# Kernel tuning notes

Hardware: AMD Instinct MI355X
Metric: run time of the kernel (lower is better)

The kernel has to match this reference:

```python
import jax, jax.numpy as jnp
import numpy as np

B, S, D = 2, 2048, 1024
H, HD = 16, 64  # num_attention_heads, attention_head_size


def setup_inputs() -> dict:
    key = jax.random.key(0)
    ks = jax.random.split(key, 8)
    std = 0.02
    return {
        "hidden_states": jax.random.normal(ks[0], (B, S, D), dtype=jnp.float32),
        "attention_mask": jnp.zeros((B, 1, 1, S), dtype=jnp.float32),
        "Wq": jax.random.normal(ks[1], (D, D), dtype=jnp.float32) * std,
        "bq": jnp.zeros((D,), dtype=jnp.float32),
        "Wk": jax.random.normal(ks[2], (D, D), dtype=jnp.float32) * std,
        "bk": jnp.zeros((D,), dtype=jnp.float32),
        "Wv": jax.random.normal(ks[3], (D, D), dtype=jnp.float32) * std,
        "bv": jnp.zeros((D,), dtype=jnp.float32),
    }


def reference(hidden_states, attention_mask, Wq, bq, Wk, bk, Wv, bv):
    b, s, d = hidden_states.shape

    def split_heads(x):  # [b,s,D] -> [b,H,s,HD]
        return x.reshape(b, s, H, HD).transpose(0, 2, 1, 3)

    q = split_heads(hidden_states @ Wq + bq)
    k = split_heads(hidden_states @ Wk + bk)
    v = split_heads(hidden_states @ Wv + bv)

    scores = jnp.einsum("bhqd,bhkd->bhqk", q, k) / jnp.sqrt(jnp.float32(HD))
    scores = scores + attention_mask  # additive mask, broadcast [b,1,1,s]
    probs = jax.nn.softmax(scores, axis=-1)  # dropout is identity at inference
    ctx = jnp.einsum("bhqk,bhkd->bhqd", probs, v)
    out = ctx.transpose(0, 2, 1, 3).reshape(b, s, d)
    return out
```

## Files before the change

### kernel.cpp

```cpp
#include <hip/hip_runtime.h>
#include <math.h>

#define CB 2
#define CS 2048
#define CD 1024
#define CH 16
#define CHD 64
#define CM (CB*CS)

#define QSCALE 0.18033688f
#define LOG2E  1.44269504f
#define BLOG   40.0f

typedef unsigned short u16;
using bf16x8 = __attribute__((ext_vector_type(8))) short;
using u16x8  = __attribute__((ext_vector_type(8))) unsigned short;
using f32x4  = __attribute__((ext_vector_type(4))) float;

__device__ __forceinline__ u16 f2bf(float f) {
    unsigned int u = __float_as_uint(f);
    u = (u + 0x7FFFu + ((u >> 16) & 1u)) >> 16;
    return (u16)u;
}

__device__ __forceinline__ unsigned cvt_pk_bf16(float lo, float hi) {
    unsigned r;
    asm("v_cvt_pk_bf16_f32 %0, %1, %2" : "=v"(r) : "v"(lo), "v"(hi));
    return r;
}

__device__ __forceinline__ void load_lds16(const u16* g, u16* l) {
    __builtin_amdgcn_global_load_lds(
        (const __attribute__((address_space(1))) unsigned int*)g,
        (__attribute__((address_space(3))) unsigned int*)l, 16, 0, 0);
}

__global__ __launch_bounds__(256)
void convert_x(const float* __restrict__ X, u16* __restrict__ Xb)
{
    size_t i = ((size_t)blockIdx.x * 256 + threadIdx.x) * 8;
    float4 v0 = *(const float4*)(X + i);
    float4 v1 = *(const float4*)(X + i + 4);
    u16x8 o;
    o[0] = f2bf(v0.x); o[1] = f2bf(v0.y); o[2] = f2bf(v0.z); o[3] = f2bf(v0.w);
    o[4] = f2bf(v1.x); o[5] = f2bf(v1.y); o[6] = f2bf(v1.z); o[7] = f2bf(v1.w);
    *(u16x8*)(Xb + i) = o;
}

__global__ __launch_bounds__(256)
void convert_wt(const float* __restrict__ Wq, const float* __restrict__ Wk,
                const float* __restrict__ Wv, u16* __restrict__ Wt)
{
    const int z = blockIdx.z;
    const float* W = (z == 0) ? Wq : (z == 1) ? Wk : Wv;
    const float sc = (z == 0) ? QSCALE : 1.0f;
    u16* Wo = Wt + (size_t)z * CD * CD;

    __shared__ u16 T[64][72];
    const int k0 = blockIdx.x << 6;
    const int n0 = blockIdx.y << 6;
    const int tid = threadIdx.x;

    #pragma unroll
    for (int it = 0; it < 4; ++it) {
        int r = (tid >> 4) + (it << 4);
        int c = (tid & 15) << 2;
        float4 v = *(const float4*)(W + (size_t)(k0 + r) * CD + n0 + c);
        T[c + 0][r] = f2bf(v.x * sc);
        T[c + 1][r] = f2bf(v.y * sc);
        T[c + 2][r] = f2bf(v.z * sc);
        T[c + 3][r] = f2bf(v.w * sc);
    }
    __syncthreads();
    #pragma unroll
    for (int it = 0; it < 2; ++it) {
        int cc = tid + (it << 8);
        int n  = cc >> 3;
        int ch = (cc & 7) << 3;
        *(uint4*)(Wo + (size_t)(n0 + n) * CD + k0 + ch) = *(const uint4*)&T[n][ch];
    }
}

__global__ __launch_bounds__(256, 3)
void qkv_gemm_mfma(const u16* __restrict__ Xb, const u16* __restrict__ Wt,
                   const float* __restrict__ bq, const float* __restrict__ bk,
                   const float* __restrict__ bv,
                   u16* __restrict__ Qb, u16* __restrict__ Kb,
                   u16* __restrict__ Vt)
{
    const int z = blockIdx.z;
    const u16* W = Wt + (size_t)z * CD * CD;
    const float* bias = (z == 0) ? bq : (z == 1) ? bk : bv;
    const float bscale = (z == 0) ? QSCALE : 1.0f;

    __shared__ u16 smem[16384];
    u16* As = smem;
    u16* Bs = smem + 8192;

    const int tid  = threadIdx.x;
    const int w    = tid >> 6;
    const int l    = tid & 63;
    const int l15  = l & 15;
    const int quad = l >> 4;
    const int wm   = w >> 1;
    const int wn   = w & 1;

    const int row0 = blockIdx.x << 7;
    const int n0   = blockIdx.y << 7;

    f32x4 acc[4][4];
    #pragma unroll
    for (int mi = 0; mi < 4; ++mi)
        #pragma unroll
        for (int nt = 0; nt < 4; ++nt)
            acc[mi][nt] = (f32x4){0.f, 0.f, 0.f, 0.f};

    const u16* Ag = Xb + (size_t)row0 * CD;
    const u16* Bg = W  + (size_t)n0   * CD;
    const int lr8 = l >> 3;
    const int ls  = l & 7;
    const int lg  = (ls ^ lr8) << 3;
    const int q7  = l15 & 7;

    for (int k0 = 0; k0 < CD; k0 += 64) {
        __syncthreads();
        #pragma unroll
        for (int i = 0; i < 4; ++i) {
            int r = w * 32 + 8 * i + lr8;
            load_lds16(Ag + (size_t)r * CD + k0 + lg, As + (size_t)(w * 32 + 8 * i) * 64);
            load_lds16(Bg + (size_t)r * CD + k0 + lg, Bs + (size_t)(w * 32 + 8 * i) * 64);
        }
        __syncthreads();

        #pragma unroll
        for (int kk = 0; kk < 2; ++kk) {
            bf16x8 af[4], bfr[4];
            #pragma unroll
            for (int mi = 0; mi < 4; ++mi)
                af[mi] = *(const bf16x8*)
                    &As[(wm * 64 + mi * 16 + l15) * 64 + (((kk * 4 + quad) ^ q7) << 3)];
            #pragma unroll
            for (int nt = 0; nt < 4; ++nt)
                bfr[nt] = *(const bf16x8*)
                    &Bs[(wn * 64 + nt * 16 + l15) * 64 + (((kk * 4 + quad) ^ q7) << 3)];
            #pragma unroll
            for (int mi = 0; mi < 4; ++mi)
                #pragma unroll
                for (int nt = 0; nt < 4; ++nt)
                    acc[mi][nt] = __builtin_amdgcn_mfma_f32_16x16x32_bf16(
                        af[mi], bfr[nt], acc[mi][nt], 0, 0, 0);
        }
    }

    __syncthreads();

    if (z < 2) {
        u16* Og = (z == 0) ? Qb : Kb;
        float bb[4];
        #pragma unroll
        for (int nt = 0; nt < 4; ++nt)
            bb[nt] = bias[n0 + wn * 64 + nt * 16 + l15] * bscale;

        u16 (*Ct)[136] = (u16(*)[136])smem;
        #pragma unroll
        for (int mh = 0; mh < 2; ++mh) {
            if (wm == mh) {
                #pragma unroll
                for (int nt = 0; nt < 4; ++nt)
                    #pragma unroll
                    for (int mi = 0; mi < 4; ++mi)
                        #pragma unroll
                        for (int r = 0; r < 4; ++r)
                            Ct[mi * 16 + quad * 4 + r][wn * 64 + nt * 16 + l15] =
                                f2bf(acc[mi][nt][r] + bb[nt]);
            }
            __syncthreads();
            #pragma unroll
            for (int it = 0; it < 4; ++it) {
                int c  = tid + (it << 8);
                int rl = c >> 4;
                int ck = c & 15;
                uint4 d = *(const uint4*)&Ct[rl][ck * 8];
                int gcol = n0 + ck * 8;
                int h = gcol >> 6, hd = gcol & 63;
                int m = row0 + mh * 64 + rl;
                int b = m >> 11, s = m & (CS - 1);
                *(uint4*)(Og + ((size_t)(b * CH + h) * CS + s) * CHD + hd) = d;
            }
            __syncthreads();
        }
    } else {
        u16 (*Ct)[136] = (u16(*)[136])smem;
        #pragma unroll
        for (int nh = 0; nh < 2; ++nh) {
            if (wn == nh) {
                #pragma unroll
                for (int nt = 0; nt < 4; ++nt) {
                    int col = n0 + nh * 64 + nt * 16 + l15;
                    float bb = bias[col];
                    #pragma unroll
                    for (int mi = 0; mi < 4; ++mi)
                        #pragma unroll
                        for (int r = 0; r < 4; ++r) {
                            int ml = wm * 64 + mi * 16 + quad * 4 + r;
                            Ct[nt * 16 + l15][ml] = f2bf(acc[mi][nt][r] + bb);
                        }
                }
            }
            __syncthreads();
            #pragma unroll
            for (int it = 0; it < 4; ++it) {
                int c   = tid + (it << 8);
                int dvl = c >> 4;
                int ch  = c & 15;
                uint4 vdat = *(const uint4*)&Ct[dvl][ch * 8];
                int col = n0 + nh * 64 + dvl;
                int h   = col >> 6;
                int dv  = col & 63;
                int m0  = row0 + ch * 8;
                int b   = m0 >> 11;
                int s0  = m0 & (CS - 1);
                *(uint4*)(Vt + (((size_t)(b * CH + h)) * CHD + dv) * CS + s0) = vdat;
            }
            __syncthreads();
        }
    }
}

__global__ __launch_bounds__(512, 4)
void attn_mfma(const u16* __restrict__ Qg, const u16* __restrict__ Kg,
               const u16* __restrict__ Vtg, const float* __restrict__ mask,
               float* __restrict__ out)
{
    __shared__ u16 smem[32768];
    u16* KstB = smem;
    u16* VstB = smem + 8192;
    u16* PlB  = smem + 16384;

    const int flat = blockIdx.y * 16 + blockIdx.x;
    const int nf   = ((flat & 7) << 6) + (flat >> 3);
    const int q0   = (nf & 15) << 7;
    const int bh   = nf >> 4;
    const int b    = bh >> 4;
    const int h    = bh & 15;

    const int tid = threadIdx.x;
    const int w    = tid >> 6;
    const int qh   = w & 3;
    const int kh   = w >> 2;
    const int l    = tid & 63;
    const int l15  = l & 15;
    const int quad = l >> 4;
    const int q7   = l15 & 7;
    const int lr8  = l >> 3;
    const int lg   = ((l & 7) ^ lr8) << 3;

    const u16* Qp     = Qg  + (size_t)bh * CS * CHD;
    const u16* Kph    = Kg  + (size_t)bh * CS * CHD + ((size_t)(kh << 10)) * CHD;
    const u16* Vph    = Vtg + (size_t)bh * CHD * CS + (kh << 10);
    const float* mrh  = mask + (size_t)b * CS + (kh << 10);

    u16* Kst = KstB + kh * 4096;
    u16* Vst = VstB + kh * 4096;
    u16* Pw  = PlB  + w * 2048;

    bf16x8 qf[2][2];
    #pragma unroll
    for (int nq = 0; nq < 2; ++nq)
        #pragma unroll
        for (int hh = 0; hh < 2; ++hh)
            qf[nq][hh] = *(const bf16x8*)(
                Qp + (size_t)(q0 + qh * 32 + nq * 16 + l15) * CHD + hh * 32 + quad * 8);

    float lsum[2] = {0.f, 0.f};
    f32x4 O[2][4];
    #pragma unroll
    for (int nq = 0; nq < 2; ++nq)
        #pragma unroll
        for (int dt = 0; dt < 4; ++dt)
            O[nq][dt] = (f32x4){0.f, 0.f, 0.f, 0.f};

    for (int kt = 0; kt < 16; ++kt) {
        const int k0 = kt << 6;
        __syncthreads();
        #pragma unroll
        for (int i = 0; i < 2; ++i) {
            int rl = qh * 16 + 8 * i;
            load_lds16(Kph + (size_t)(k0 + rl + lr8) * CHD + lg, &Kst[rl * 64]);
            load_lds16(Vph + (size_t)(rl + lr8) * CS + k0 + lg,  &Vst[rl * 64]);
        }
        __syncthreads();

        bf16x8 kf[4][2];
        #pragma unroll
        for (int mt = 0; mt < 4; ++mt)
            #pragma unroll
            for (int hh = 0; hh < 2; ++hh)
                kf[mt][hh] = *(const bf16x8*)
                    &Kst[(mt * 16 + l15) * 64 + (((hh * 4 + quad) ^ q7) << 3)];

        f32x4 mc[4];
        #pragma unroll
        for (int mt = 0; mt < 4; ++mt) {
            f32x4 mv = *(const f32x4*)(mrh + k0 + mt * 16 + quad * 4);
            #pragma unroll
            for (int r = 0; r < 4; ++r)
                mc[mt][r] = fmaf(mv[r], LOG2E, -BLOG);
        }

        #pragma unroll
        for (int nq = 0; nq < 2; ++nq) {
            f32x4 st[4];
            #pragma unroll
            for (int mt = 0; mt < 4; ++mt) {
                f32x4 c0 = mc[mt];
                c0 = __builtin_amdgcn_mfma_f32_16x16x32_bf16(kf[mt][0], qf[nq][0], c0, 0, 0, 0);
                st[mt] = __builtin_amdgcn_mfma_f32_16x16x32_bf16(kf[mt][1], qf[nq][1], c0, 0, 0, 0);
            }
            float rs = lsum[nq];
            #pragma unroll
            for (int mt = 0; mt < 4; ++mt) {
                #pragma unroll
                for (int r = 0; r < 4; ++r) {
                    st[mt][r] = exp2f(st[mt][r]);
                    rs += st[mt][r];
                }
                int g = 2 * mt + (quad >> 1);
                int addr = (nq * 16 + l15) * 64 + ((g ^ q7) << 3) + ((quad & 1) << 2);
                uint2 d;
                d.x = cvt_pk_bf16(st[mt][0], st[mt][1]);
                d.y = cvt_pk_bf16(st[mt][2], st[mt][3]);
                *(uint2*)&Pw[addr] = d;
            }
            lsum[nq] = rs;
        }

        bf16x8 pf[2][2];
        #pragma unroll
        for (int nq = 0; nq < 2; ++nq)
            #pragma unroll
            for (int hh = 0; hh < 2; ++hh)
                pf[nq][hh] = *(const bf16x8*)
                    &Pw[(nq * 16 + l15) * 64 + (((hh * 4 + quad) ^ q7) << 3)];

        bf16x8 vf[4][2];
        #pragma unroll
        for (int dt = 0; dt < 4; ++dt)
            #pragma unroll
            for (int hh = 0; hh < 2; ++hh)
                vf[dt][hh] = *(const bf16x8*)
                    &Vst[(dt * 16 + l15) * 64 + (((hh * 4 + quad) ^ q7) << 3)];

        #pragma unroll
        for (int nq = 0; nq < 2; ++nq)
            #pragma unroll
            for (int dt = 0; dt < 4; ++dt) {
                O[nq][dt] = __builtin_amdgcn_mfma_f32_16x16x32_bf16(
                    pf[nq][0], vf[dt][0], O[nq][dt], 0, 0, 0);
                O[nq][dt] = __builtin_amdgcn_mfma_f32_16x16x32_bf16(
                    pf[nq][1], vf[dt][1], O[nq][dt], 0, 0, 0);
            }
    }

    #pragma unroll
    for (int nq = 0; nq < 2; ++nq) {
        lsum[nq] += __shfl_xor(lsum[nq], 16);
        lsum[nq] += __shfl_xor(lsum[nq], 32);
    }

    __syncthreads();
    float* ob   = (float*)smem;
    float* lbuf = (float*)PlB;

    if (kh == 1) {
        float* obw = ob + qh * 2048;
        #pragma unroll
        for (int nq = 0; nq < 2; ++nq)
            #pragma unroll
            for (int dt = 0; dt < 4; ++dt)
                #pragma unroll
                for (int r = 0; r < 4; ++r)
                    obw[(nq * 16 + quad * 4 + r) * 64 + dt * 16 + l15] = O[nq][dt][r];
        if (quad == 0) {
            lbuf[qh * 32 + l15]      = lsum[0];
            lbuf[qh * 32 + 16 + l15] = lsum[1];
        }
    }
    __syncthreads();

    if (kh == 0) {
        const float* obw = ob + qh * 2048;
        #pragma unroll
        for (int nq = 0; nq < 2; ++nq) {
            float inv = 1.0f / (lsum[nq] + lbuf[qh * 32 + nq * 16 + l15]);
            #pragma unroll
            for (int r = 0; r < 4; ++r) {
                float invr = __shfl(inv, quad * 4 + r);
                int q = q0 + qh * 32 + nq * 16 + quad * 4 + r;
                float* orow = out + ((size_t)b * CS + q) * CD + h * CHD;
                #pragma unroll
                for (int dt = 0; dt < 4; ++dt)
                    orow[dt * 16 + l15] =
                        (O[nq][dt][r] + obw[(nq * 16 + quad * 4 + r) * 64 + dt * 16 + l15]) * invr;
            }
        }
    }
}

extern "C" void kernel_launch(void* const* d_in, const int* in_sizes, int n_in,
                              void* d_out, int out_size, void* d_ws, size_t ws_size,
                              hipStream_t stream)
{
    const float* X    = (const float*)d_in[0];
    const float* mask = (const float*)d_in[1];
    const float* Wq   = (const float*)d_in[2];
    const float* bq   = (const float*)d_in[3];
    const float* Wk   = (const float*)d_in[4];
    const float* bk   = (const float*)d_in[5];
    const float* Wv   = (const float*)d_in[6];
    const float* bv   = (const float*)d_in[7];
    float* out = (float*)d_out;

    char* ws = (char*)d_ws;
    u16* Xb = (u16*)(ws);
    u16* Wt = (u16*)(ws + ((size_t)8  << 20));
    u16* Qb = (u16*)(ws + ((size_t)14 << 20));
    u16* Kb = (u16*)(ws + ((size_t)22 << 20));
    u16* Vt = (u16*)(ws + ((size_t)30 << 20));

    convert_x<<<CM * CD / (256 * 8), 256, 0, stream>>>(X, Xb);
    convert_wt<<<dim3(16, 16, 3), 256, 0, stream>>>(Wq, Wk, Wv, Wt);
    qkv_gemm_mfma<<<dim3(CM / 128, CD / 128, 3), 256, 0, stream>>>(
        Xb, Wt, bq, bk, bv, Qb, Kb, Vt);
    attn_mfma<<<dim3(CS / 128, CB * CH), 512, 0, stream>>>(Qb, Kb, Vt, mask, out);
}
```

Measured before the change: 183.0 us.

## Compute softmax row sums with MFMA against ones and prefetch mask tiles

Replaces the per-lane scalar accumulation of exponentiated scores with an MFMA of the bf16 P fragments against a ones vector, so row sums come out of the matrix unit. The final sums are then gathered with shuffles instead of xor reductions. It also manually unrolls the key loop by two with ping-pong mask registers, so the next tile's mask is loaded one iteration early. The MFMA path adds four extra MFMAs per tile and sums the bf16-rounded probabilities instead of the fp32 values, which slightly changes the normalisation numerics.

```diff
diff --git a/kernel.cpp b/kernel.cpp
--- a/kernel.cpp
+++ b/kernel.cpp
@@ -227,6 +227,84 @@
     }
 }
 
+
+#define AT_TILE(KT, MVC, MVN)                                                 \
+    {                                                                         \
+        const int k0 = (KT) << 6;                                             \
+        __syncthreads();                                                      \
+        _Pragma("unroll")                                                     \
+        for (int i = 0; i < 2; ++i) {                                         \
+            int rl = qh * 16 + 8 * i;                                         \
+            load_lds16(Kph + (size_t)(k0 + rl + lr8) * CHD + lg, &Kst[rl * 64]); \
+            load_lds16(Vph + (size_t)(rl + lr8) * CS + k0 + lg,  &Vst[rl * 64]); \
+        }                                                                     \
+        __syncthreads();                                                      \
+        bf16x8 kf[4][2];                                                      \
+        _Pragma("unroll")                                                     \
+        for (int mt = 0; mt < 4; ++mt)                                        \
+            _Pragma("unroll")                                                 \
+            for (int hh = 0; hh < 2; ++hh)                                    \
+                kf[mt][hh] = *(const bf16x8*)                                 \
+                    &Kst[(mt * 16 + l15) * 64 + (((hh * 4 + quad) ^ q7) << 3)]; \
+        const int kn = ((KT) + 1) & 15;                                       \
+        _Pragma("unroll")                                                     \
+        for (int mt = 0; mt < 4; ++mt)                                        \
+            MVN[mt] = *(const f32x4*)(mrh + (kn << 6) + mt * 16 + quad * 4);  \
+        f32x4 mc[4];                                                          \
+        _Pragma("unroll")                                                     \
+        for (int mt = 0; mt < 4; ++mt)                                        \
+            _Pragma("unroll")                                                 \
+            for (int r = 0; r < 4; ++r)                                       \
+                mc[mt][r] = fmaf(MVC[mt][r], LOG2E, -BLOG);                   \
+        _Pragma("unroll")                                                     \
+        for (int nq = 0; nq < 2; ++nq) {                                      \
+            f32x4 st[4];                                                      \
+            _Pragma("unroll")                                                 \
+            for (int mt = 0; mt < 4; ++mt) {                                  \
+                f32x4 c0 = mc[mt];                                            \
+                c0 = __builtin_amdgcn_mfma_f32_16x16x32_bf16(kf[mt][0], qf[nq][0], c0, 0, 0, 0); \
+                st[mt] = __builtin_amdgcn_mfma_f32_16x16x32_bf16(kf[mt][1], qf[nq][1], c0, 0, 0, 0); \
+            }                                                                 \
+            _Pragma("unroll")                                                 \
+            for (int mt = 0; mt < 4; ++mt) {                                  \
+                _Pragma("unroll")                                             \
+                for (int r = 0; r < 4; ++r) st[mt][r] = exp2f(st[mt][r]);     \
+                int g = 2 * mt + (quad >> 1);                                 \
+                int addr = (nq * 16 + l15) * 64 + ((g ^ q7) << 3) + ((quad & 1) << 2); \
+                uint2 d;                                                      \
+                d.x = cvt_pk_bf16(st[mt][0], st[mt][1]);                      \
+                d.y = cvt_pk_bf16(st[mt][2], st[mt][3]);                      \
+                *(uint2*)&Pw[addr] = d;                                       \
+            }                                                                 \
+        }                                                                     \
+        bf16x8 pf[2][2];                                                      \
+        _Pragma("unroll")                                                     \
+        for (int nq = 0; nq < 2; ++nq)                                        \
+            _Pragma("unroll")                                                 \
+            for (int hh = 0; hh < 2; ++hh)                                    \
+                pf[nq][hh] = *(const bf16x8*)                                 \
+                    &Pw[(nq * 16 + l15) * 64 + (((hh * 4 + quad) ^ q7) << 3)]; \
+        bf16x8 vf[4][2];                                                      \
+        _Pragma("unroll")                                                     \
+        for (int dt = 0; dt < 4; ++dt)                                        \
+            _Pragma("unroll")                                                 \
+            for (int hh = 0; hh < 2; ++hh)                                    \
+                vf[dt][hh] = *(const bf16x8*)                                 \
+                    &Vst[(dt * 16 + l15) * 64 + (((hh * 4 + quad) ^ q7) << 3)]; \
+        _Pragma("unroll")                                                     \
+        for (int nq = 0; nq < 2; ++nq) {                                      \
+            Lq[nq] = __builtin_amdgcn_mfma_f32_16x16x32_bf16(pf[nq][0], ones, Lq[nq], 0, 0, 0); \
+            Lq[nq] = __builtin_amdgcn_mfma_f32_16x16x32_bf16(pf[nq][1], ones, Lq[nq], 0, 0, 0); \
+            _Pragma("unroll")                                                 \
+            for (int dt = 0; dt < 4; ++dt) {                                  \
+                O[nq][dt] = __builtin_amdgcn_mfma_f32_16x16x32_bf16(          \
+                    pf[nq][0], vf[dt][0], O[nq][dt], 0, 0, 0);                \
+                O[nq][dt] = __builtin_amdgcn_mfma_f32_16x16x32_bf16(          \
+                    pf[nq][1], vf[dt][1], O[nq][dt], 0, 0, 0);                \
+            }                                                                 \
+        }                                                                     \
+    }
+
 __global__ __launch_bounds__(512, 4)
 void attn_mfma(const u16* __restrict__ Qg, const u16* __restrict__ Kg,
                const u16* __restrict__ Vtg, const float* __restrict__ mask,
@@ -272,7 +350,12 @@
             qf[nq][hh] = *(const bf16x8*)(
                 Qp + (size_t)(q0 + qh * 32 + nq * 16 + l15) * CHD + hh * 32 + quad * 8);
 
-    float lsum[2] = {0.f, 0.f};
+    const short ob16 = (short)0x3F80;
+    const bf16x8 ones = {ob16, ob16, ob16, ob16, ob16, ob16, ob16, ob16};
+
+    f32x4 Lq[2];
+    Lq[0] = (f32x4){0.f, 0.f, 0.f, 0.f};
+    Lq[1] = (f32x4){0.f, 0.f, 0.f, 0.f};
     f32x4 O[2][4];
     #pragma unroll
     for (int nq = 0; nq < 2; ++nq)
@@ -280,92 +363,28 @@
         for (int dt = 0; dt < 4; ++dt)
             O[nq][dt] = (f32x4){0.f, 0.f, 0.f, 0.f};
 
-    for (int kt = 0; kt < 16; ++kt) {
-        const int k0 = kt << 6;
-        __syncthreads();
-        #pragma unroll
-        for (int i = 0; i < 2; ++i) {
-            int rl = qh * 16 + 8 * i;
-            load_lds16(Kph + (size_t)(k0 + rl + lr8) * CHD + lg, &Kst[rl * 64]);
-            load_lds16(Vph + (size_t)(rl + lr8) * CS + k0 + lg,  &Vst[rl * 64]);
-        }
-        __syncthreads();
-
-        bf16x8 kf[4][2];
-        #pragma unroll
-        for (int mt = 0; mt < 4; ++mt)
-            #pragma unroll
-            for (int hh = 0; hh < 2; ++hh)
-                kf[mt][hh] = *(const bf16x8*)
-                    &Kst[(mt * 16 + l15) * 64 + (((hh * 4 + quad) ^ q7) << 3)];
-
-        f32x4 mc[4];
-        #pragma unroll
-        for (int mt = 0; mt < 4; ++mt) {
-            f32x4 mv = *(const f32x4*)(mrh + k0 + mt * 16 + quad * 4);
-            #pragma unroll
-            for (int r = 0; r < 4; ++r)
-                mc[mt][r] = fmaf(mv[r], LOG2E, -BLOG);
-        }
-
-        #pragma unroll
-        for (int nq = 0; nq < 2; ++nq) {
-            f32x4 st[4];
-            #pragma unroll
-            for (int mt = 0; mt < 4; ++mt) {
-                f32x4 c0 = mc[mt];
-                c0 = __builtin_amdgcn_mfma_f32_16x16x32_bf16(kf[mt][0], qf[nq][0], c0, 0, 0, 0);
-                st[mt] = __builtin_amdgcn_mfma_f32_16x16x32_bf16(kf[mt][1], qf[nq][1], c0, 0, 0, 0);
-            }
-            float rs = lsum[nq];
-            #pragma unroll
-            for (int mt = 0; mt < 4; ++mt) {
-                #pragma unroll
-                for (int r = 0; r < 4; ++r) {
-                    st[mt][r] = exp2f(st[mt][r]);
-                    rs += st[mt][r];
-                }
-                int g = 2 * mt + (quad >> 1);
-                int addr = (nq * 16 + l15) * 64 + ((g ^ q7) << 3) + ((quad & 1) << 2);
-                uint2 d;
-                d.x = cvt_pk_bf16(st[mt][0], st[mt][1]);
-                d.y = cvt_pk_bf16(st[mt][2], st[mt][3]);
-                *(uint2*)&Pw[addr] = d;
-            }
-            lsum[nq] = rs;
-        }
-
-        bf16x8 pf[2][2];
-        #pragma unroll
-        for (int nq = 0; nq < 2; ++nq)
-            #pragma unroll
-            for (int hh = 0; hh < 2; ++hh)
-                pf[nq][hh] = *(const bf16x8*)
-                    &Pw[(nq * 16 + l15) * 64 + (((hh * 4 + quad) ^ q7) << 3)];
-
-        bf16x8 vf[4][2];
-        #pragma unroll
-        for (int dt = 0; dt < 4; ++dt)
-            #pragma unroll
-            for (int hh = 0; hh < 2; ++hh)
-                vf[dt][hh] = *(const bf16x8*)
-                    &Vst[(dt * 16 + l15) * 64 + (((hh * 4 + quad) ^ q7) << 3)];
-
-        #pragma unroll
-        for (int nq = 0; nq < 2; ++nq)
-            #pragma unroll
-            for (int dt = 0; dt < 4; ++dt) {
-                O[nq][dt] = __builtin_amdgcn_mfma_f32_16x16x32_bf16(
-                    pf[nq][0], vf[dt][0], O[nq][dt], 0, 0, 0);
-                O[nq][dt] = __builtin_amdgcn_mfma_f32_16x16x32_bf16(
-                    pf[nq][1], vf[dt][1], O[nq][dt], 0, 0, 0);
-            }
-    }
-
+    f32x4 mvA[4], mvB[4];
+    #pragma unroll
+    for (int mt = 0; mt < 4; ++mt)
+        mvA[mt] = *(const f32x4*)(mrh + mt * 16 + quad * 4);
+
+    #pragma unroll 1
+    for (int kt = 0; kt < 16; kt += 2) {
+        AT_TILE(kt,     mvA, mvB)
+        AT_TILE(kt + 1, mvB, mvA)
+    }
+
+    float lsum[2];
     #pragma unroll
     for (int nq = 0; nq < 2; ++nq) {
-        lsum[nq] += __shfl_xor(lsum[nq], 16);
-        lsum[nq] += __shfl_xor(lsum[nq], 32);
+        const int src = (l15 >> 2) << 4;
+        float s0 = __shfl(Lq[nq][0], src);
+        float s1 = __shfl(Lq[nq][1], src);
+        float s2 = __shfl(Lq[nq][2], src);
+        float s3 = __shfl(Lq[nq][3], src);
+        float lo = (l15 & 1) ? s1 : s0;
+        float hi2 = (l15 & 1) ? s3 : s2;
+        lsum[nq] = (l15 & 2) ? hi2 : lo;
     }
 
     __syncthreads();
```

After: 185.1 us. No clear change (+1.1%).
